# Kernel optimization log

Hardware: AMD Instinct MI355X
Metric: run time of the kernel (lower is better)

## Reference

```python
import jax, jax.numpy as jnp
import numpy as np

H = 128  # hidden_dim

def setup_inputs() -> dict:
    key = jax.random.key(0)
    ks = jax.random.split(key, 8)
    B, S = 32, 512
    return {
        "CNN_output": jax.random.normal(ks[0], (B, 4 * S, H), jnp.float32),
        "gaz_input": jax.random.normal(ks[1], (B, S, 128), jnp.float32),
        "gaz_input_back": jax.random.normal(ks[2], (B, S, 128), jnp.float32),
        "global_matrix": jax.random.normal(ks[3], (B, S, H), jnp.float32),
        "exper_input": jax.random.normal(ks[4], (B, S, H), jnp.float32),
        "W_cat": jax.random.normal(ks[5], (3 * H, 16 * H), jnp.float32) * (1.0 / np.sqrt(3 * H)),
        "b_cat": jnp.zeros((16 * H,), jnp.float32),
        "W_exp": jax.random.normal(ks[6], (H, 12 * H), jnp.float32) * (1.0 / np.sqrt(H)),
        "b_exp": jnp.zeros((12 * H,), jnp.float32),
    }


def _diag_gather(y, B, S, width):
    # y: [B, 4*S, 4*width]; for seq-block j pick columns j*width:(j+1)*width
    y = y.reshape(B, 4, S, 4, width)
    j = jnp.arange(4)
    y = y[:, j, :, j, :]              # [4, B, S, width]
    return jnp.transpose(y, (1, 0, 2, 3)).reshape(B, 4 * S, width)


def reference(CNN_output, gaz_input, gaz_input_back, global_matrix, exper_input,
              W_cat, b_cat, W_exp, b_exp):
    B, S4, _ = CNN_output.shape
    S = S4 // 4
    gaz = jnp.concatenate([gaz_input, gaz_input_back, gaz_input, gaz_input_back], axis=1)
    gm = jnp.tile(global_matrix, (1, 4, 1))
    exp_rep = jnp.tile(exper_input, (1, 4, 1))
    cat_in = jnp.concatenate([CNN_output, gaz, gm], axis=2)      # [B, 4S, 3H]
    cat_gates = _diag_gather(cat_in @ W_cat + b_cat, B, S, 4 * H)  # [B, 4S, 4H]
    exper_gates = _diag_gather(exp_rep @ W_exp + b_exp, B, S, 3 * H)  # [B, 4S, 3H]
    new_state = jnp.tanh(cat_gates[:, :, :H])
    gates = jax.nn.sigmoid(cat_gates[:, :, H:] + exper_gates)
    gates = jax.nn.softmax(gates.reshape(B, S4, 3, H), axis=2)
    state_cat = jnp.stack([new_state, CNN_output, exp_rep], axis=2)  # [B, 4S, 3, H]
    layer_output = jnp.sum(gates * state_cat, axis=2)                # [B, 4S, H]
    return tuple(layer_output[:, i * S:(i + 1) * S] for i in range(4))
```

## Files before the change

kernel.cpp:

```cpp
#include <hip/hip_runtime.h>

typedef unsigned short u16;
typedef unsigned int u32;
typedef short bf16x8 __attribute__((ext_vector_type(8)));
typedef float f32x4 __attribute__((ext_vector_type(4)));

#define HH 128

__device__ __forceinline__ u16 f2bf(float f) {
  u32 u = __float_as_uint(f);
  u += 0x7fffu + ((u >> 16) & 1u);
  return (u16)(u >> 16);
}
__device__ __forceinline__ u32 pack2(float a, float b) {
  return (u32)f2bf(a) | ((u32)f2bf(b) << 16);
}
__device__ __forceinline__ float bf2f(u16 h) {
  return __uint_as_float(((u32)h) << 16);
}

__global__ __launch_bounds__(256) void prep_w(const float* __restrict__ Wcat,
                                              const float* __restrict__ Wexp,
                                              u16* __restrict__ Wc) {
  const int bx = blockIdx.x;
  const int nt = bx & 7;
  const int kc = (bx >> 3) & 15;
  const int q = bx >> 7;
  __shared__ u16 T[32 * 72];

  const int tid = threadIdx.x;
  const int r = tid >> 3;
  const int c8 = (tid & 7) * 8;
  float v[8];
  if (kc < 12) {
    const float* src =
        Wcat + (size_t)(kc * 32 + r) * 2048 + q * 512 + nt * 64 + c8;
    float4 a = *(const float4*)src;
    float4 b = *(const float4*)(src + 4);
    v[0] = a.x; v[1] = a.y; v[2] = a.z; v[3] = a.w;
    v[4] = b.x; v[5] = b.y; v[6] = b.z; v[7] = b.w;
  } else if (nt >= 2) {
    const float* src = Wexp + (size_t)((kc - 12) * 32 + r) * 1536 + q * 384 +
                       nt * 64 + c8 - 128;
    float4 a = *(const float4*)src;
    float4 b = *(const float4*)(src + 4);
    v[0] = a.x; v[1] = a.y; v[2] = a.z; v[3] = a.w;
    v[4] = b.x; v[5] = b.y; v[6] = b.z; v[7] = b.w;
  } else {
#pragma unroll
    for (int j = 0; j < 8; ++j) v[j] = 0.f;
  }
  uint4 pk;
  pk.x = pack2(v[0], v[1]);
  pk.y = pack2(v[2], v[3]);
  pk.z = pack2(v[4], v[5]);
  pk.w = pack2(v[6], v[7]);
  *(uint4*)&T[r * 72 + c8] = pk;
  __syncthreads();

  const int p = tid & 3;
  const int nl = tid >> 2;
  const int lq = p ^ (nl & 3) ^ ((nl >> 2) & 3);
  u16 w[8];
#pragma unroll
  for (int j = 0; j < 8; ++j) w[j] = T[(lq * 8 + j) * 72 + nl];
  uint4 o;
  o.x = (u32)w[0] | ((u32)w[1] << 16);
  o.y = (u32)w[2] | ((u32)w[3] << 16);
  o.z = (u32)w[4] | ((u32)w[5] << 16);
  o.w = (u32)w[6] | ((u32)w[7] << 16);
  const size_t idx = ((size_t)((q * 16 + kc) * 512) + nt * 64 + nl) * 4 + p;
  ((uint4*)Wc)[idx] = o;
}

__global__ __launch_bounds__(512, 4) void fused_gate(
    const float* __restrict__ CNN, const float* __restrict__ gaz,
    const float* __restrict__ gazb, const float* __restrict__ gm,
    const float* __restrict__ exper, const u16* __restrict__ Wc,
    const float* __restrict__ bcat, const float* __restrict__ bexp,
    float* __restrict__ out) {
  __shared__ u16 Abuf[16 * 64 * 32];

  const int tid = threadIdx.x;
  const int lane = tid & 63;
  const int wave = tid >> 6;
  const int bx = blockIdx.x;
  const int tile = bx & 7;
  const int grp = bx >> 3;
  const int b = grp >> 2;
  const int q = grp & 3;
  const int s_base = tile * 64;

  const int sel = wave >> 1;
  const float* src_w =
      (sel == 0) ? CNN + (size_t)(b * 2048 + q * 512 + s_base) * HH
      : (sel == 1) ? (((q & 1) ? gazb : gaz) + (size_t)(b * 512 + s_base) * HH)
      : (sel == 2) ? gm + (size_t)(b * 512 + s_base) * HH
                   : exper + (size_t)(b * 512 + s_base) * HH;
#pragma unroll
  for (int t = 0; t < 8; ++t) {
    const int s = t * 64 + lane;
    const int row = (wave & 1) * 32 + (s >> 4);
    const int oct = s & 15;
    const float* sp = src_w + (size_t)row * HH + oct * 8;
    float4 f0 = *(const float4*)sp;
    float4 f1 = *(const float4*)(sp + 4);
    uint4 pk;
    pk.x = pack2(f0.x, f0.y);
    pk.y = pack2(f0.z, f0.w);
    pk.z = pack2(f1.x, f1.y);
    pk.w = pack2(f1.z, f1.w);
    const int kc = sel * 4 + (oct >> 2);
    const int o = oct & 3;
    const int ph = o ^ ((row & 3) ^ ((row >> 2) & 3)) ^ sel;
    *(uint4*)&Abuf[(kc * 64 + row) * 32 + ph * 8] = pk;
  }
  __syncthreads();

  const int l15 = lane & 15;
  const int quad = lane >> 4;
  const int sl = (l15 & 3) ^ ((l15 >> 2) & 3);
  const int physB = quad ^ sl;

  const char* __restrict__ Wq = (const char*)(Wc + (size_t)q * 262144);
  u32 offb[4];
#pragma unroll
  for (int gg = 0; gg < 4; ++gg) {
    const int n = gg * 128 + wave * 16 + l15;
    offb[gg] = (u32)((n * 4 + physB) * 16);
  }

  f32x4 acc[4][4];
#pragma unroll
  for (int rt = 0; rt < 4; ++rt)
#pragma unroll
    for (int gg = 0; gg < 4; ++gg) acc[rt][gg] = (f32x4)0.f;

  bf16x8 bcur[4], bnxt[4];
#pragma unroll
  for (int gg = 0; gg < 4; ++gg)
    bcur[gg] = *(const bf16x8*)(Wq + offb[gg]);

#pragma unroll
  for (int kc = 0; kc < 16; ++kc) {
    if (kc < 15) {
      const u32 kb = (u32)(kc + 1) * 32768u;
#pragma unroll
      for (int gg = 0; gg < 4; ++gg)
        bnxt[gg] = *(const bf16x8*)(Wq + (kb + offb[gg]));
    }
    const int pa = (quad ^ sl ^ (kc >> 2)) * 8;
    const u16* ab = &Abuf[(kc * 64 + l15) * 32 + pa];
    bf16x8 af0 = *(const bf16x8*)(ab);
    bf16x8 af1 = *(const bf16x8*)(ab + 16 * 32);
    __builtin_amdgcn_s_setprio(1);
#pragma unroll
    for (int gg = 0; gg < 4; ++gg)
      acc[0][gg] = __builtin_amdgcn_mfma_f32_16x16x32_bf16(af0, bcur[gg],
                                                           acc[0][gg], 0, 0, 0);
#pragma unroll
    for (int gg = 0; gg < 4; ++gg)
      acc[1][gg] = __builtin_amdgcn_mfma_f32_16x16x32_bf16(af1, bcur[gg],
                                                           acc[1][gg], 0, 0, 0);
    __builtin_amdgcn_s_setprio(0);
    bf16x8 af2 = *(const bf16x8*)(ab + 32 * 32);
    bf16x8 af3 = *(const bf16x8*)(ab + 48 * 32);
    __builtin_amdgcn_s_setprio(1);
#pragma unroll
    for (int gg = 0; gg < 4; ++gg)
      acc[2][gg] = __builtin_amdgcn_mfma_f32_16x16x32_bf16(af2, bcur[gg],
                                                           acc[2][gg], 0, 0, 0);
#pragma unroll
    for (int gg = 0; gg < 4; ++gg)
      acc[3][gg] = __builtin_amdgcn_mfma_f32_16x16x32_bf16(af3, bcur[gg],
                                                           acc[3][gg], 0, 0, 0);
    __builtin_amdgcn_s_setprio(0);
#pragma unroll
    for (int gg = 0; gg < 4; ++gg) bcur[gg] = bnxt[gg];
  }

  const float* bcq = bcat + q * 512;
  const float* beq = bexp + q * 384;
  const size_t outbase = (size_t)((q * 32 + b) * 512 + s_base) * HH;
  const int h = wave * 16 + l15;
  const float bc0 = bcq[h];
  const float bc1 = bcq[128 + h];
  const float bc2 = bcq[256 + h];
  const float bc3 = bcq[384 + h];
  const float be1 = beq[h];
  const float be2 = beq[128 + h];
  const float be3 = beq[256 + h];
  const int kcc = h >> 5;
  const int kce = 12 + (h >> 5);
  const int oh = (h >> 3) & 3;
  const int he = h & 7;
#pragma unroll
  for (int rt = 0; rt < 4; ++rt) {
#pragma unroll
    for (int r = 0; r < 4; ++r) {
      const int row = rt * 16 + quad * 4 + r;
      const int srw = (row & 3) ^ ((row >> 2) & 3);
      const float cnn = bf2f(Abuf[(kcc * 64 + row) * 32 + (oh ^ srw) * 8 + he]);
      const float ex =
          bf2f(Abuf[(kce * 64 + row) * 32 + (oh ^ srw ^ 3) * 8 + he]);
      const float c0 = acc[rt][0][r] + bc0;
      const float p1 = acc[rt][1][r] + bc1 + be1;
      const float p2 = acc[rt][2][r] + bc2 + be2;
      const float p3 = acc[rt][3][r] + bc3 + be3;
      const float e2c = __expf(2.f * c0);
      const float ns = 1.f - 2.f * __builtin_amdgcn_rcpf(e2c + 1.f);
      const float g1 = __builtin_amdgcn_rcpf(1.f + __expf(-p1));
      const float g2 = __builtin_amdgcn_rcpf(1.f + __expf(-p2));
      const float g3 = __builtin_amdgcn_rcpf(1.f + __expf(-p3));
      const float e1 = __expf(g1);
      const float e2 = __expf(g2);
      const float e3 = __expf(g3);
      const float inv = __builtin_amdgcn_rcpf(e1 + e2 + e3);
      out[outbase + (size_t)row * HH + h] = (e1 * ns + e2 * cnn + e3 * ex) * inv;
    }
  }
}

extern "C" void kernel_launch(void* const* d_in, const int* in_sizes, int n_in,
                              void* d_out, int out_size, void* d_ws, size_t ws_size,
                              hipStream_t stream) {
  const float* CNN = (const float*)d_in[0];
  const float* gaz = (const float*)d_in[1];
  const float* gazb = (const float*)d_in[2];
  const float* gm = (const float*)d_in[3];
  const float* exper = (const float*)d_in[4];
  const float* Wcat = (const float*)d_in[5];
  const float* bcat = (const float*)d_in[6];
  const float* Wexp = (const float*)d_in[7];
  const float* bexp = (const float*)d_in[8];
  u16* Wc = (u16*)d_ws;

  prep_w<<<512, 256, 0, stream>>>(Wcat, Wexp, Wc);
  fused_gate<<<1024, 512, 0, stream>>>(CNN, gaz, gazb, gm, exper, Wc, bcat,
                                       bexp, (float*)d_out);
}
```

Measured before the change: 152.6 us.

## Double M-tile to 128 rows and overlap second-half A staging with MFMA

Each block now handles 128 sequence rows instead of 64, halving the grid and reusing each loaded weight fragment across twice as many MFMA tiles. The A operand is staged in two halves: the first half (CNN and gaz) is converted up front, and the second half (gm and exper) is loaded and converted while the first K-chunks are computed. Float-to-bf16 packing uses the hardware v_cvt_pk_bf16_f32 instruction, and the CNN residual is now read from global memory in full fp32 rather than from the bf16 shared copy. The cost is more accumulator registers (occupancy hint dropped to 2 blocks per CU), an extra barrier, and fewer blocks for load balancing.

After: 150.7 us. Within noise of the previous version (-1.3%).

```diff
diff --git a/kernel.cpp b/kernel.cpp
--- a/kernel.cpp
+++ b/kernel.cpp
@@ -17,6 +17,11 @@
 }
 __device__ __forceinline__ float bf2f(u16 h) {
   return __uint_as_float(((u32)h) << 16);
+}
+__device__ __forceinline__ u32 cvtpk(float lo, float hi) {
+  u32 r;
+  asm("v_cvt_pk_bf16_f32 %0, %1, %2" : "=v"(r) : "v"(lo), "v"(hi));
+  return r;
 }
 
 __global__ __launch_bounds__(256) void prep_w(const float* __restrict__ Wcat,
@@ -73,47 +78,49 @@
   ((uint4*)Wc)[idx] = o;
 }
 
-__global__ __launch_bounds__(512, 4) void fused_gate(
+__global__ __launch_bounds__(512, 2) void fused_gate(
     const float* __restrict__ CNN, const float* __restrict__ gaz,
     const float* __restrict__ gazb, const float* __restrict__ gm,
     const float* __restrict__ exper, const u16* __restrict__ Wc,
     const float* __restrict__ bcat, const float* __restrict__ bexp,
     float* __restrict__ out) {
-  __shared__ u16 Abuf[16 * 64 * 32];
+  __shared__ u16 Abuf[2][8 * 128 * 32];
 
   const int tid = threadIdx.x;
   const int lane = tid & 63;
   const int wave = tid >> 6;
   const int bx = blockIdx.x;
-  const int tile = bx & 7;
-  const int grp = bx >> 3;
+  const int tile = bx & 3;
+  const int grp = bx >> 2;
   const int b = grp >> 2;
   const int q = grp & 3;
-  const int s_base = tile * 64;
-
-  const int sel = wave >> 1;
-  const float* src_w =
-      (sel == 0) ? CNN + (size_t)(b * 2048 + q * 512 + s_base) * HH
-      : (sel == 1) ? (((q & 1) ? gazb : gaz) + (size_t)(b * 512 + s_base) * HH)
-      : (sel == 2) ? gm + (size_t)(b * 512 + s_base) * HH
-                   : exper + (size_t)(b * 512 + s_base) * HH;
+  const int s_base = tile * 128;
+
+  const int sel2 = wave >> 2;
+  const int rg = wave & 3;
+  const float* srcA0 =
+      (sel2 == 0) ? CNN + (size_t)(b * 2048 + q * 512 + s_base) * HH
+                  : (((q & 1) ? gazb : gaz) + (size_t)(b * 512 + s_base) * HH);
+  const float* srcA1 =
+      (sel2 == 0) ? gm + (size_t)(b * 512 + s_base) * HH
+                  : exper + (size_t)(b * 512 + s_base) * HH;
+
 #pragma unroll
   for (int t = 0; t < 8; ++t) {
-    const int s = t * 64 + lane;
-    const int row = (wave & 1) * 32 + (s >> 4);
-    const int oct = s & 15;
-    const float* sp = src_w + (size_t)row * HH + oct * 8;
+    const int srow = rg * 32 + t * 4 + (lane >> 4);
+    const int oct = lane & 15;
+    const float* sp = srcA0 + (size_t)srow * HH + oct * 8;
     float4 f0 = *(const float4*)sp;
     float4 f1 = *(const float4*)(sp + 4);
     uint4 pk;
-    pk.x = pack2(f0.x, f0.y);
-    pk.y = pack2(f0.z, f0.w);
-    pk.z = pack2(f1.x, f1.y);
-    pk.w = pack2(f1.z, f1.w);
-    const int kc = sel * 4 + (oct >> 2);
-    const int o = oct & 3;
-    const int ph = o ^ ((row & 3) ^ ((row >> 2) & 3)) ^ sel;
-    *(uint4*)&Abuf[(kc * 64 + row) * 32 + ph * 8] = pk;
+    pk.x = cvtpk(f0.x, f0.y);
+    pk.y = cvtpk(f0.z, f0.w);
+    pk.z = cvtpk(f1.x, f1.y);
+    pk.w = cvtpk(f1.z, f1.w);
+    const int kcl = sel2 * 4 + (oct >> 2);
+    const int srw = (srow & 3) ^ ((srow >> 2) & 3);
+    const int ph = (oct & 3) ^ srw ^ ((kcl >> 2) & 3);
+    *(uint4*)&Abuf[0][(kcl * 128 + srow) * 32 + ph * 8] = pk;
   }
   __syncthreads();
 
@@ -121,7 +128,6 @@
   const int quad = lane >> 4;
   const int sl = (l15 & 3) ^ ((l15 >> 2) & 3);
   const int physB = quad ^ sl;
-
   const char* __restrict__ Wq = (const char*)(Wc + (size_t)q * 262144);
   u32 offb[4];
 #pragma unroll
@@ -130,51 +136,92 @@
     offb[gg] = (u32)((n * 4 + physB) * 16);
   }
 
-  f32x4 acc[4][4];
-#pragma unroll
-  for (int rt = 0; rt < 4; ++rt)
+  f32x4 acc[8][4];
+#pragma unroll
+  for (int rt = 0; rt < 8; ++rt)
 #pragma unroll
     for (int gg = 0; gg < 4; ++gg) acc[rt][gg] = (f32x4)0.f;
 
   bf16x8 bcur[4], bnxt[4];
 #pragma unroll
+  for (int gg = 0; gg < 4; ++gg) bcur[gg] = *(const bf16x8*)(Wq + offb[gg]);
+
+#pragma unroll
+  for (int kc = 0; kc < 8; ++kc) {
+    const int srow = rg * 32 + kc * 4 + (lane >> 4);
+    const int oct = lane & 15;
+    const float* sp = srcA1 + (size_t)srow * HH + oct * 8;
+    float4 f0 = *(const float4*)sp;
+    float4 f1 = *(const float4*)(sp + 4);
+    if (kc < 7) {
+      const u32 kb = (u32)(kc + 1) * 32768u;
+#pragma unroll
+      for (int gg = 0; gg < 4; ++gg)
+        bnxt[gg] = *(const bf16x8*)(Wq + (kb + offb[gg]));
+    }
+    const int pa = (quad ^ sl ^ ((kc >> 2) & 3)) * 8;
+    const u16* ab = &Abuf[0][(kc * 128 + l15) * 32 + pa];
+#pragma unroll
+    for (int pr = 0; pr < 4; ++pr) {
+      bf16x8 afa = *(const bf16x8*)(ab + (2 * pr) * 16 * 32);
+      bf16x8 afb = *(const bf16x8*)(ab + (2 * pr + 1) * 16 * 32);
+      __builtin_amdgcn_s_setprio(1);
+#pragma unroll
+      for (int gg = 0; gg < 4; ++gg)
+        acc[2 * pr][gg] = __builtin_amdgcn_mfma_f32_16x16x32_bf16(
+            afa, bcur[gg], acc[2 * pr][gg], 0, 0, 0);
+#pragma unroll
+      for (int gg = 0; gg < 4; ++gg)
+        acc[2 * pr + 1][gg] = __builtin_amdgcn_mfma_f32_16x16x32_bf16(
+            afb, bcur[gg], acc[2 * pr + 1][gg], 0, 0, 0);
+      __builtin_amdgcn_s_setprio(0);
+    }
+    {
+      uint4 pk;
+      pk.x = cvtpk(f0.x, f0.y);
+      pk.y = cvtpk(f0.z, f0.w);
+      pk.z = cvtpk(f1.x, f1.y);
+      pk.w = cvtpk(f1.z, f1.w);
+      const int kcl = sel2 * 4 + (oct >> 2);
+      const int kcg = 8 + kcl;
+      const int srw = (srow & 3) ^ ((srow >> 2) & 3);
+      const int ph = (oct & 3) ^ srw ^ ((kcg >> 2) & 3);
+      *(uint4*)&Abuf[1][(kcl * 128 + srow) * 32 + ph * 8] = pk;
+    }
+#pragma unroll
+    for (int gg = 0; gg < 4; ++gg) bcur[gg] = bnxt[gg];
+  }
+
+  __syncthreads();
+
+#pragma unroll
   for (int gg = 0; gg < 4; ++gg)
-    bcur[gg] = *(const bf16x8*)(Wq + offb[gg]);
-
-#pragma unroll
-  for (int kc = 0; kc < 16; ++kc) {
+    bcur[gg] = *(const bf16x8*)(Wq + (8u * 32768u + offb[gg]));
+#pragma unroll
+  for (int kc = 8; kc < 16; ++kc) {
     if (kc < 15) {
       const u32 kb = (u32)(kc + 1) * 32768u;
 #pragma unroll
       for (int gg = 0; gg < 4; ++gg)
         bnxt[gg] = *(const bf16x8*)(Wq + (kb + offb[gg]));
     }
-    const int pa = (quad ^ sl ^ (kc >> 2)) * 8;
-    const u16* ab = &Abuf[(kc * 64 + l15) * 32 + pa];
-    bf16x8 af0 = *(const bf16x8*)(ab);
-    bf16x8 af1 = *(const bf16x8*)(ab + 16 * 32);
-    __builtin_amdgcn_s_setprio(1);
-#pragma unroll
-    for (int gg = 0; gg < 4; ++gg)
-      acc[0][gg] = __builtin_amdgcn_mfma_f32_16x16x32_bf16(af0, bcur[gg],
-                                                           acc[0][gg], 0, 0, 0);
-#pragma unroll
-    for (int gg = 0; gg < 4; ++gg)
-      acc[1][gg] = __builtin_amdgcn_mfma_f32_16x16x32_bf16(af1, bcur[gg],
-                                                           acc[1][gg], 0, 0, 0);
-    __builtin_amdgcn_s_setprio(0);
-    bf16x8 af2 = *(const bf16x8*)(ab + 32 * 32);
-    bf16x8 af3 = *(const bf16x8*)(ab + 48 * 32);
-    __builtin_amdgcn_s_setprio(1);
-#pragma unroll
-    for (int gg = 0; gg < 4; ++gg)
-      acc[2][gg] = __builtin_amdgcn_mfma_f32_16x16x32_bf16(af2, bcur[gg],
-                                                           acc[2][gg], 0, 0, 0);
-#pragma unroll
-    for (int gg = 0; gg < 4; ++gg)
-      acc[3][gg] = __builtin_amdgcn_mfma_f32_16x16x32_bf16(af3, bcur[gg],
-                                                           acc[3][gg], 0, 0, 0);
-    __builtin_amdgcn_s_setprio(0);
+    const int pa = (quad ^ sl ^ ((kc >> 2) & 3)) * 8;
+    const u16* ab = &Abuf[1][((kc - 8) * 128 + l15) * 32 + pa];
+#pragma unroll
+    for (int pr = 0; pr < 4; ++pr) {
+      bf16x8 afa = *(const bf16x8*)(ab + (2 * pr) * 16 * 32);
+      bf16x8 afb = *(const bf16x8*)(ab + (2 * pr + 1) * 16 * 32);
+      __builtin_amdgcn_s_setprio(1);
+#pragma unroll
+      for (int gg = 0; gg < 4; ++gg)
+        acc[2 * pr][gg] = __builtin_amdgcn_mfma_f32_16x16x32_bf16(
+            afa, bcur[gg], acc[2 * pr][gg], 0, 0, 0);
+#pragma unroll
+      for (int gg = 0; gg < 4; ++gg)
+        acc[2 * pr + 1][gg] = __builtin_amdgcn_mfma_f32_16x16x32_bf16(
+            afb, bcur[gg], acc[2 * pr + 1][gg], 0, 0, 0);
+      __builtin_amdgcn_s_setprio(0);
+    }
 #pragma unroll
     for (int gg = 0; gg < 4; ++gg) bcur[gg] = bnxt[gg];
   }
@@ -190,19 +237,20 @@
   const float be1 = beq[h];
   const float be2 = beq[128 + h];
   const float be3 = beq[256 + h];
-  const int kcc = h >> 5;
-  const int kce = 12 + (h >> 5);
+  const int slot_e = 4 + (h >> 5);
   const int oh = (h >> 3) & 3;
   const int he = h & 7;
-#pragma unroll
-  for (int rt = 0; rt < 4; ++rt) {
+  const float* cnnb =
+      CNN + (size_t)(b * 2048 + q * 512 + s_base) * HH + h;
+#pragma unroll
+  for (int rt = 0; rt < 8; ++rt) {
 #pragma unroll
     for (int r = 0; r < 4; ++r) {
       const int row = rt * 16 + quad * 4 + r;
       const int srw = (row & 3) ^ ((row >> 2) & 3);
-      const float cnn = bf2f(Abuf[(kcc * 64 + row) * 32 + (oh ^ srw) * 8 + he]);
+      const float cnn = cnnb[(size_t)row * HH];
       const float ex =
-          bf2f(Abuf[(kce * 64 + row) * 32 + (oh ^ srw ^ 3) * 8 + he]);
+          bf2f(Abuf[1][(slot_e * 128 + row) * 32 + (oh ^ srw ^ 3) * 8 + he]);
       const float c0 = acc[rt][0][r] + bc0;
       const float p1 = acc[rt][1][r] + bc1 + be1;
       const float p2 = acc[rt][2][r] + bc2 + be2;
@@ -236,6 +284,6 @@
   u16* Wc = (u16*)d_ws;
 
   prep_w<<<512, 256, 0, stream>>>(Wcat, Wexp, Wc);
-  fused_gate<<<1024, 512, 0, stream>>>(CNN, gaz, gazb, gm, exper, Wc, bcat,
-                                       bexp, (float*)d_out);
-}
+  fused_gate<<<512, 512, 0, stream>>>(CNN, gaz, gazb, gm, exper, Wc, bcat,
+                                      bexp, (float*)d_out);
+}
```

## Stage weight tiles through double-buffered LDS with direct global-to-LDS loads

Applied to the files above, without the earlier changes.

Weight (B) fragments are no longer loaded per wave straight from global memory into registers. They are now copied cooperatively with global_load_lds into a double-buffered shared-memory buffer and read from LDS each K step, with manual vmcnt waits and barriers around every iteration. The A-tile conversion also switches to a hardware packed bf16 convert instruction. The change adds 64 KB of LDS per block and lowers the occupancy hint from 4 to 2, and the two block-wide barriers per K step may cost more than the redundant global loads they remove.

Result: slower. 177.4 us (+16.2%).

```diff
diff --git a/kernel.cpp b/kernel.cpp
--- a/kernel.cpp
+++ b/kernel.cpp
@@ -17,6 +17,11 @@
 }
 __device__ __forceinline__ float bf2f(u16 h) {
   return __uint_as_float(((u32)h) << 16);
+}
+__device__ __forceinline__ u32 cvtpk(float lo, float hi) {
+  u32 r;
+  asm("v_cvt_pk_bf16_f32 %0, %1, %2" : "=v"(r) : "v"(lo), "v"(hi));
+  return r;
 }
 
 __global__ __launch_bounds__(256) void prep_w(const float* __restrict__ Wcat,
@@ -73,13 +78,14 @@
   ((uint4*)Wc)[idx] = o;
 }
 
-__global__ __launch_bounds__(512, 4) void fused_gate(
+__global__ __launch_bounds__(512, 2) void fused_gate(
     const float* __restrict__ CNN, const float* __restrict__ gaz,
     const float* __restrict__ gazb, const float* __restrict__ gm,
     const float* __restrict__ exper, const u16* __restrict__ Wc,
     const float* __restrict__ bcat, const float* __restrict__ bexp,
     float* __restrict__ out) {
   __shared__ u16 Abuf[16 * 64 * 32];
+  __shared__ u16 Bbuf[2 * 16384];
 
   const int tid = threadIdx.x;
   const int lane = tid & 63;
@@ -106,22 +112,20 @@
     float4 f0 = *(const float4*)sp;
     float4 f1 = *(const float4*)(sp + 4);
     uint4 pk;
-    pk.x = pack2(f0.x, f0.y);
-    pk.y = pack2(f0.z, f0.w);
-    pk.z = pack2(f1.x, f1.y);
-    pk.w = pack2(f1.z, f1.w);
+    pk.x = cvtpk(f0.x, f0.y);
+    pk.y = cvtpk(f0.z, f0.w);
+    pk.z = cvtpk(f1.x, f1.y);
+    pk.w = cvtpk(f1.z, f1.w);
     const int kc = sel * 4 + (oct >> 2);
     const int o = oct & 3;
     const int ph = o ^ ((row & 3) ^ ((row >> 2) & 3)) ^ sel;
     *(uint4*)&Abuf[(kc * 64 + row) * 32 + ph * 8] = pk;
   }
-  __syncthreads();
 
   const int l15 = lane & 15;
   const int quad = lane >> 4;
   const int sl = (l15 & 3) ^ ((l15 >> 2) & 3);
   const int physB = quad ^ sl;
-
   const char* __restrict__ Wq = (const char*)(Wc + (size_t)q * 262144);
   u32 offb[4];
 #pragma unroll
@@ -130,53 +134,74 @@
     offb[gg] = (u32)((n * 4 + physB) * 16);
   }
 
+  const char* gB = Wq + (size_t)(wave * 1024 + lane * 16);
+  u16* bw0 = &Bbuf[wave * 512];
+  u16* bw1 = &Bbuf[16384 + wave * 512];
+
   f32x4 acc[4][4];
 #pragma unroll
   for (int rt = 0; rt < 4; ++rt)
 #pragma unroll
     for (int gg = 0; gg < 4; ++gg) acc[rt][gg] = (f32x4)0.f;
 
-  bf16x8 bcur[4], bnxt[4];
-#pragma unroll
-  for (int gg = 0; gg < 4; ++gg)
-    bcur[gg] = *(const bf16x8*)(Wq + offb[gg]);
+#pragma unroll
+  for (int i = 0; i < 4; ++i)
+    __builtin_amdgcn_global_load_lds((const u32*)(gB + i * 8192),
+                                     (u32*)(bw0 + i * 4096), 16, 0, 0);
+  __syncthreads();
 
 #pragma unroll
   for (int kc = 0; kc < 16; ++kc) {
     if (kc < 15) {
-      const u32 kb = (u32)(kc + 1) * 32768u;
-#pragma unroll
-      for (int gg = 0; gg < 4; ++gg)
-        bnxt[gg] = *(const bf16x8*)(Wq + (kb + offb[gg]));
+      const char* g = gB + (size_t)(kc + 1) * 32768;
+      u16* d = ((kc + 1) & 1) ? bw1 : bw0;
+#pragma unroll
+      for (int i = 0; i < 4; ++i)
+        __builtin_amdgcn_global_load_lds((const u32*)(g + i * 8192),
+                                         (u32*)(d + i * 4096), 16, 0, 0);
     }
+    if (kc < 15)
+      asm volatile("s_waitcnt vmcnt(4)" ::: "memory");
+    else
+      asm volatile("s_waitcnt vmcnt(0)" ::: "memory");
+    __builtin_amdgcn_sched_barrier(0);
+    __builtin_amdgcn_s_barrier();
+    __builtin_amdgcn_sched_barrier(0);
+
+    const u16* bb = &Bbuf[(kc & 1) * 16384];
+    bf16x8 bf0 = *(const bf16x8*)((const char*)bb + offb[0]);
+    bf16x8 bf1 = *(const bf16x8*)((const char*)bb + offb[1]);
+    bf16x8 bf2 = *(const bf16x8*)((const char*)bb + offb[2]);
+    bf16x8 bf3 = *(const bf16x8*)((const char*)bb + offb[3]);
     const int pa = (quad ^ sl ^ (kc >> 2)) * 8;
     const u16* ab = &Abuf[(kc * 64 + l15) * 32 + pa];
     bf16x8 af0 = *(const bf16x8*)(ab);
     bf16x8 af1 = *(const bf16x8*)(ab + 16 * 32);
     __builtin_amdgcn_s_setprio(1);
-#pragma unroll
-    for (int gg = 0; gg < 4; ++gg)
-      acc[0][gg] = __builtin_amdgcn_mfma_f32_16x16x32_bf16(af0, bcur[gg],
-                                                           acc[0][gg], 0, 0, 0);
-#pragma unroll
-    for (int gg = 0; gg < 4; ++gg)
-      acc[1][gg] = __builtin_amdgcn_mfma_f32_16x16x32_bf16(af1, bcur[gg],
-                                                           acc[1][gg], 0, 0, 0);
+    acc[0][0] = __builtin_amdgcn_mfma_f32_16x16x32_bf16(af0, bf0, acc[0][0], 0, 0, 0);
+    acc[0][1] = __builtin_amdgcn_mfma_f32_16x16x32_bf16(af0, bf1, acc[0][1], 0, 0, 0);
+    acc[0][2] = __builtin_amdgcn_mfma_f32_16x16x32_bf16(af0, bf2, acc[0][2], 0, 0, 0);
+    acc[0][3] = __builtin_amdgcn_mfma_f32_16x16x32_bf16(af0, bf3, acc[0][3], 0, 0, 0);
+    acc[1][0] = __builtin_amdgcn_mfma_f32_16x16x32_bf16(af1, bf0, acc[1][0], 0, 0, 0);
+    acc[1][1] = __builtin_amdgcn_mfma_f32_16x16x32_bf16(af1, bf1, acc[1][1], 0, 0, 0);
+    acc[1][2] = __builtin_amdgcn_mfma_f32_16x16x32_bf16(af1, bf2, acc[1][2], 0, 0, 0);
+    acc[1][3] = __builtin_amdgcn_mfma_f32_16x16x32_bf16(af1, bf3, acc[1][3], 0, 0, 0);
     __builtin_amdgcn_s_setprio(0);
     bf16x8 af2 = *(const bf16x8*)(ab + 32 * 32);
     bf16x8 af3 = *(const bf16x8*)(ab + 48 * 32);
     __builtin_amdgcn_s_setprio(1);
-#pragma unroll
-    for (int gg = 0; gg < 4; ++gg)
-      acc[2][gg] = __builtin_amdgcn_mfma_f32_16x16x32_bf16(af2, bcur[gg],
-                                                           acc[2][gg], 0, 0, 0);
-#pragma unroll
-    for (int gg = 0; gg < 4; ++gg)
-      acc[3][gg] = __builtin_amdgcn_mfma_f32_16x16x32_bf16(af3, bcur[gg],
-                                                           acc[3][gg], 0, 0, 0);
+    acc[2][0] = __builtin_amdgcn_mfma_f32_16x16x32_bf16(af2, bf0, acc[2][0], 0, 0, 0);
+    acc[2][1] = __builtin_amdgcn_mfma_f32_16x16x32_bf16(af2, bf1, acc[2][1], 0, 0, 0);
+    acc[2][2] = __builtin_amdgcn_mfma_f32_16x16x32_bf16(af2, bf2, acc[2][2], 0, 0, 0);
+    acc[2][3] = __builtin_amdgcn_mfma_f32_16x16x32_bf16(af2, bf3, acc[2][3], 0, 0, 0);
+    acc[3][0] = __builtin_amdgcn_mfma_f32_16x16x32_bf16(af3, bf0, acc[3][0], 0, 0, 0);
+    acc[3][1] = __builtin_amdgcn_mfma_f32_16x16x32_bf16(af3, bf1, acc[3][1], 0, 0, 0);
+    acc[3][2] = __builtin_amdgcn_mfma_f32_16x16x32_bf16(af3, bf2, acc[3][2], 0, 0, 0);
+    acc[3][3] = __builtin_amdgcn_mfma_f32_16x16x32_bf16(af3, bf3, acc[3][3], 0, 0, 0);
     __builtin_amdgcn_s_setprio(0);
-#pragma unroll
-    for (int gg = 0; gg < 4; ++gg) bcur[gg] = bnxt[gg];
+    __builtin_amdgcn_sched_barrier(0);
+    __builtin_amdgcn_s_barrier();
+    __builtin_amdgcn_sched_barrier(0);
   }
 
   const float* bcq = bcat + q * 512;
```
